# Kernel tuning notes

Measured on AMD Instinct MI355X. Metric: run time of the kernel, lower is better.

Reference implementation:

```python
import jax, jax.numpy as jnp
import numpy as np

N_HEAD = 8
LN_EPS = 1e-6


def setup_inputs() -> dict:
    key = jax.random.key(0)
    ks = jax.random.split(key, 6)
    B, S, D = 4, 2048, 256  # D = hidden_size*2 = input_dim
    sc = 1.0 / np.sqrt(D)
    return {
        "inputs": jax.random.normal(ks[0], (B, S, D), jnp.float32),
        "Wq": jax.random.normal(ks[1], (D, D), jnp.float32) * sc,
        "Wk": jax.random.normal(ks[2], (D, D), jnp.float32) * sc,
        "Wv": jax.random.normal(ks[3], (D, D), jnp.float32) * sc,
        "Wf": jax.random.normal(ks[4], (D, D), jnp.float32) * sc,
        "bf": jnp.zeros((D,), jnp.float32),
        "gamma": jnp.ones((D,), jnp.float32),
        "beta": jnp.zeros((D,), jnp.float32),
    }


def reference(inputs, Wq, Wk, Wv, Wf, bf, gamma, beta):
    B, S, D = inputs.shape
    H = N_HEAD
    dh = D // H
    # Projections (torch Linear: x @ W.T), no bias for Q/K/V
    Q = (inputs @ Wq.T).reshape(B, S, H, dh)
    K = (inputs @ Wk.T).reshape(B, S, H, dh)
    V = (inputs @ Wv.T).reshape(B, S, H, dh)
    # NOTE: original scales by sqrt(K.shape[1]) == sqrt(seq_len), not sqrt(dh)
    scale = 1.0 / jnp.sqrt(jnp.float32(S)).astype(inputs.dtype)
    scores = jnp.einsum("bqhd,bkhd->bhqk", Q, K) * scale  # [B,H,S,S]
    attn = jax.nn.softmax(scores, axis=-1)
    out = jnp.einsum("bhqk,bkhd->bqhd", attn, V).reshape(B, S, D)
    out = out @ Wf.T + bf
    # residual + LayerNorm(eps=1e-6)
    x = inputs + out
    mu = jnp.mean(x, axis=-1, keepdims=True)
    var = jnp.mean(jnp.square(x - mu), axis=-1, keepdims=True)
    return (x - mu) * jax.lax.rsqrt(var + LN_EPS) * gamma + beta
```

## Files before the change

### kernel.cpp

```cpp
#include <hip/hip_runtime.h>
#include <hip/hip_bf16.h>

typedef __attribute__((ext_vector_type(8))) short short8;
typedef __attribute__((ext_vector_type(4))) float f32x4;
typedef __attribute__((ext_vector_type(16))) float f32x16;

#define DEVI __device__ __forceinline__

DEVI unsigned short f2bf(float f) {
  union { float f; unsigned int u; } v; v.f = f;
  unsigned int r = v.u + 0x7fffu + ((v.u >> 16) & 1u);
  return (unsigned short)(r >> 16);
}

#define SB 4
#define SS 2048
#define SD 256
#define SH 8
#define SDH 32
#define SM 8192

#define QSCALE 0.0318793654f

#define XBF_OFF 0
#define W_OFF   (SM * SD)
#define Q_OFF   (W_OFF + 4 * SD * SD)
#define K_OFF   (Q_OFF + SM * SD)
#define VT_OFF  (K_OFF + SM * SD)
#define AO_OFF  (VT_OFF + SM * SD)

__global__ __launch_bounds__(256) void convert_k(
    const float* __restrict__ X, const float* __restrict__ Wq,
    const float* __restrict__ Wk, const float* __restrict__ Wv,
    const float* __restrict__ Wf, unsigned short* __restrict__ ws) {
  const int XN = SM * SD;
  const int WN = SD * SD;
  int i4 = (blockIdx.x * 256 + threadIdx.x) * 4;
  const float* src; unsigned short* dst; int idx;
  if (i4 < XN)             { src = X;  dst = ws + XBF_OFF;      idx = i4; }
  else if (i4 < XN + WN)   { src = Wq; dst = ws + W_OFF;        idx = i4 - XN; }
  else if (i4 < XN + 2*WN) { src = Wk; dst = ws + W_OFF + WN;   idx = i4 - XN - WN; }
  else if (i4 < XN + 3*WN) { src = Wv; dst = ws + W_OFF + 2*WN; idx = i4 - XN - 2*WN; }
  else if (i4 < XN + 4*WN) { src = Wf; dst = ws + W_OFF + 3*WN; idx = i4 - XN - 3*WN; }
  else return;
  float4 v = *reinterpret_cast<const float4*>(src + idx);
  unsigned short o[4] = { f2bf(v.x), f2bf(v.y), f2bf(v.z), f2bf(v.w) };
  *reinterpret_cast<uint2*>(dst + idx) = *reinterpret_cast<const uint2*>(o);
}

__global__ __launch_bounds__(256) void qkv_k(const unsigned short* __restrict__ ws_c,
                                             unsigned short* __restrict__ ws) {
  __shared__ __align__(16) unsigned short Atile[128][72];
  __shared__ __align__(16) unsigned short Btile[128][72];
  const unsigned short* Xb = ws_c + XBF_OFF;
  const unsigned short* Wall = ws_c + W_OFF;
  int tid = threadIdx.x, w = tid >> 6, lane = tid & 63, g = lane >> 4, r = lane & 15;
  int m0 = blockIdx.x * 128, n0 = blockIdx.y * 128;
  int wr = (w >> 1) * 64, wc = (w & 1) * 64;
  f32x4 acc[4][4] = {};
  int srow = tid >> 3, scol = (tid & 7) * 8;
  for (int k0 = 0; k0 < SD; k0 += 64) {
    short8 a[4], b[4];
#pragma unroll
    for (int p = 0; p < 4; ++p) {
      a[p] = *reinterpret_cast<const short8*>(Xb + (m0 + srow + p * 32) * SD + k0 + scol);
      b[p] = *reinterpret_cast<const short8*>(Wall + (n0 + srow + p * 32) * SD + k0 + scol);
    }
    __syncthreads();
#pragma unroll
    for (int p = 0; p < 4; ++p) {
      *reinterpret_cast<short8*>(&Atile[srow + p * 32][scol]) = a[p];
      *reinterpret_cast<short8*>(&Btile[srow + p * 32][scol]) = b[p];
    }
    __syncthreads();
#pragma unroll
    for (int ks = 0; ks < 2; ++ks) {
      short8 af[4], bf[4];
#pragma unroll
      for (int i = 0; i < 4; ++i)
        af[i] = *reinterpret_cast<const short8*>(&Atile[wr + i * 16 + r][ks * 32 + g * 8]);
#pragma unroll
      for (int j = 0; j < 4; ++j)
        bf[j] = *reinterpret_cast<const short8*>(&Btile[wc + j * 16 + r][ks * 32 + g * 8]);
#pragma unroll
      for (int i = 0; i < 4; ++i)
#pragma unroll
        for (int j = 0; j < 4; ++j)
          acc[i][j] = __builtin_amdgcn_mfma_f32_16x16x32_bf16(af[i], bf[j], acc[i][j], 0, 0, 0);
    }
  }
  int z = n0 >> 8;
  int nbase = n0 & 255;
  if (z < 2) {
    unsigned short* out = ws + (z == 0 ? Q_OFF : K_OFF);
    float qs = (z == 0) ? QSCALE : 1.0f;
#pragma unroll
    for (int j = 0; j < 4; ++j) {
      int col = nbase + wc + j * 16 + r;
      int h = col >> 5, d = col & 31;
#pragma unroll
      for (int i = 0; i < 4; ++i) {
#pragma unroll
        for (int jj = 0; jj < 4; ++jj) {
          int m = m0 + wr + i * 16 + g * 4 + jj;
          int b_ = m >> 11, s = m & 2047;
          out[(((b_ << 3) + h) * SS + s) * SDH + d] = f2bf(acc[i][j][jj] * qs);
        }
      }
    }
  } else {
    unsigned short* out = ws + VT_OFF;
#pragma unroll
    for (int j = 0; j < 4; ++j) {
      int col = nbase + wc + j * 16 + r;
      int h = col >> 5, d = col & 31;
#pragma unroll
      for (int i = 0; i < 4; ++i) {
        int m = m0 + wr + i * 16 + g * 4;
        int b_ = m >> 11, s = m & 2047;
        unsigned short o4[4];
#pragma unroll
        for (int jj = 0; jj < 4; ++jj) o4[jj] = f2bf(acc[i][j][jj]);
        *reinterpret_cast<uint2*>(out + ((((b_ << 3) + h) << 5) + d) * SS + s) =
            *reinterpret_cast<const uint2*>(o4);
      }
    }
  }
}

#define TKV 128
__global__ __launch_bounds__(512, 4) void attn_k(const unsigned short* __restrict__ ws_c,
                                                 unsigned short* __restrict__ ws) {
  __shared__ __align__(16) unsigned short Kl[2][TKV][40];
  __shared__ __align__(16) unsigned short Vl[2][32][TKV + 8];
  __shared__ float OC[4][64][16];
  __shared__ float LC[4][64];
  __shared__ float Linv[4][32];
  int tid = threadIdx.x, w = tid >> 6, lane = tid & 63;
  int wg = w >> 2, wl = w & 3, gtid = tid & 255;
  int n32 = lane & 31, hi = lane >> 5;
  int wgid = ((blockIdx.x & 7) << 6) + (blockIdx.x >> 3);
  int bh = wgid >> 4, qb = wgid & 15;
  int q0 = qb * 128 + wl * 32;
  const unsigned short* Qh = ws_c + Q_OFF + bh * (SS * SDH);
  const unsigned short* Kg = ws_c + K_OFF + bh * (SS * SDH) + wg * 1024 * SDH;
  const unsigned short* Vg = ws_c + VT_OFF + bh * (SDH * SS) + wg * 1024;
  short8 qB0 = *reinterpret_cast<const short8*>(Qh + (q0 + n32) * SDH + 8 * hi);
  short8 qB1 = *reinterpret_cast<const short8*>(Qh + (q0 + n32) * SDH + 16 + 8 * hi);
  int krow = gtid >> 2, kcol = (gtid & 3) * 8;
  int vrow = gtid >> 4, vcol = (gtid & 15) * 8;
  f32x16 O = {};
  float Lacc = 0.f;
  short8 ka = *reinterpret_cast<const short8*>(Kg + krow * SDH + kcol);
  short8 kb = *reinterpret_cast<const short8*>(Kg + (64 + krow) * SDH + kcol);
  short8 va = *reinterpret_cast<const short8*>(Vg + vrow * SS + vcol);
  short8 vb = *reinterpret_cast<const short8*>(Vg + (16 + vrow) * SS + vcol);
  for (int t = 0; t < 8; ++t) {
    __syncthreads();
    *reinterpret_cast<short8*>(&Kl[wg][krow][kcol]) = ka;
    *reinterpret_cast<short8*>(&Kl[wg][64 + krow][kcol]) = kb;
    *reinterpret_cast<short8*>(&Vl[wg][vrow][vcol]) = va;
    *reinterpret_cast<short8*>(&Vl[wg][16 + vrow][vcol]) = vb;
    __syncthreads();
    if (t < 7) {
      ka = *reinterpret_cast<const short8*>(Kg + ((t + 1) * TKV + krow) * SDH + kcol);
      kb = *reinterpret_cast<const short8*>(Kg + ((t + 1) * TKV + 64 + krow) * SDH + kcol);
      va = *reinterpret_cast<const short8*>(Vg + vrow * SS + (t + 1) * TKV + vcol);
      vb = *reinterpret_cast<const short8*>(Vg + (16 + vrow) * SS + (t + 1) * TKV + vcol);
    }
#pragma unroll
    for (int s = 0; s < 4; ++s) {
      short8 kA0 = *reinterpret_cast<const short8*>(&Kl[wg][s * 32 + n32][8 * hi]);
      short8 kA1 = *reinterpret_cast<const short8*>(&Kl[wg][s * 32 + n32][16 + 8 * hi]);
      short8 vB0 = *reinterpret_cast<const short8*>(&Vl[wg][n32][s * 32 + 8 * hi]);
      short8 vB1 = *reinterpret_cast<const short8*>(&Vl[wg][n32][s * 32 + 16 + 8 * hi]);
      f32x16 acc = {};
      __builtin_amdgcn_s_setprio(1);
      acc = __builtin_amdgcn_mfma_f32_32x32x16_bf16(kA0, qB0, acc, 0, 0, 0);
      acc = __builtin_amdgcn_mfma_f32_32x32x16_bf16(kA1, qB1, acc, 0, 0, 0);
      __builtin_amdgcn_s_setprio(0);
      float p[16];
#pragma unroll
      for (int i = 0; i < 16; ++i) p[i] = __builtin_amdgcn_exp2f(acc[i]);
      float s0 = 0.f, s1 = 0.f;
#pragma unroll
      for (int i = 0; i < 8; ++i) { s0 += p[2 * i]; s1 += p[2 * i + 1]; }
      Lacc += s0 + s1;
      unsigned int pk[8];
#pragma unroll
      for (int i = 0; i < 8; ++i) {
        unsigned int rr;
        asm("v_cvt_pk_bf16_f32 %0, %1, %2" : "=v"(rr) : "v"(p[2 * i]), "v"(p[2 * i + 1]));
        pk[i] = rr;
      }
      asm("v_permlane32_swap_b32 %0, %1" : "+v"(pk[0]), "+v"(pk[2]));
      asm("v_permlane32_swap_b32 %0, %1" : "+v"(pk[1]), "+v"(pk[3]));
      asm("v_permlane32_swap_b32 %0, %1" : "+v"(pk[4]), "+v"(pk[6]));
      asm("v_permlane32_swap_b32 %0, %1" : "+v"(pk[5]), "+v"(pk[7]));
      union { unsigned int u[4]; short8 sv; } A1, A2;
      A1.u[0] = pk[0]; A1.u[1] = pk[1]; A1.u[2] = pk[2]; A1.u[3] = pk[3];
      A2.u[0] = pk[4]; A2.u[1] = pk[5]; A2.u[2] = pk[6]; A2.u[3] = pk[7];
      __builtin_amdgcn_s_setprio(1);
      O = __builtin_amdgcn_mfma_f32_32x32x16_bf16(A1.sv, vB0, O, 0, 0, 0);
      O = __builtin_amdgcn_mfma_f32_32x32x16_bf16(A2.sv, vB1, O, 0, 0, 0);
      __builtin_amdgcn_s_setprio(0);
    }
  }
  if (wg == 1) {
#pragma unroll
    for (int i = 0; i < 16; ++i) OC[wl][lane][i] = O[i];
    LC[wl][lane] = Lacc;
  }
  __syncthreads();
  if (wg == 0) {
#pragma unroll
    for (int i = 0; i < 16; ++i) O[i] += OC[wl][lane][i];
    Lacc += LC[wl][lane];
    float Lt = Lacc + __shfl_xor(Lacc, 32);
    if (lane < 32) Linv[wl][n32] = 1.0f / Lt;
    int b = bh >> 3, h = bh & 7;
    unsigned short* AO = ws + AO_OFF;
#pragma unroll
    for (int rr = 0; rr < 16; ++rr) {
      int q = (rr & 3) + 8 * (rr >> 2) + 4 * hi;
      AO[(b * SS + q0 + q) * SD + h * SDH + n32] = f2bf(O[rr] * Linv[wl][q]);
    }
  }
}

__global__ __launch_bounds__(256) void final_k(
    const unsigned short* __restrict__ ws_c, const float* __restrict__ X,
    const float* __restrict__ bfv, const float* __restrict__ gamma,
    const float* __restrict__ beta, float* __restrict__ out) {
  __shared__ __align__(16) unsigned short Al[32][72];
  __shared__ __align__(16) unsigned short Bl[256][72];
  __shared__ float Cl[32][257];
  const unsigned short* AO = ws_c + AO_OFF;
  const unsigned short* Wf = ws_c + W_OFF + 3 * (SD * SD);
  int tid = threadIdx.x, w = tid >> 6, lane = tid & 63, g = lane >> 4, r = lane & 15;
  int m0 = blockIdx.x * 32;
  f32x4 acc[2][4] = {};
  int arow = tid >> 3, acol = (tid & 7) * 8;
  for (int k0 = 0; k0 < SD; k0 += 64) {
    short8 av = *reinterpret_cast<const short8*>(AO + (m0 + arow) * SD + k0 + acol);
    short8 bv[8];
#pragma unroll
    for (int i = 0; i < 8; i++)
      bv[i] = *reinterpret_cast<const short8*>(Wf + (i * 32 + arow) * SD + k0 + acol);
    __syncthreads();
    *reinterpret_cast<short8*>(&Al[arow][acol]) = av;
#pragma unroll
    for (int i = 0; i < 8; i++)
      *reinterpret_cast<short8*>(&Bl[i * 32 + arow][acol]) = bv[i];
    __syncthreads();
#pragma unroll
    for (int ks = 0; ks < 2; ks++) {
      short8 af0 = *reinterpret_cast<const short8*>(&Al[r][ks * 32 + g * 8]);
      short8 af1 = *reinterpret_cast<const short8*>(&Al[16 + r][ks * 32 + g * 8]);
#pragma unroll
      for (int nt = 0; nt < 4; nt++) {
        short8 bb = *reinterpret_cast<const short8*>(&Bl[w * 64 + nt * 16 + r][ks * 32 + g * 8]);
        acc[0][nt] = __builtin_amdgcn_mfma_f32_16x16x32_bf16(af0, bb, acc[0][nt], 0, 0, 0);
        acc[1][nt] = __builtin_amdgcn_mfma_f32_16x16x32_bf16(af1, bb, acc[1][nt], 0, 0, 0);
      }
    }
  }
#pragma unroll
  for (int rt = 0; rt < 2; rt++)
#pragma unroll
    for (int nt = 0; nt < 4; nt++)
#pragma unroll
      for (int j = 0; j < 4; j++)
        Cl[rt * 16 + g * 4 + j][w * 64 + nt * 16 + r] = acc[rt][nt][j];
  __syncthreads();
  int row = tid >> 3, sub = tid & 7;
  int m = m0 + row;
  float x[32];
  float sum = 0.f, sumsq = 0.f;
#pragma unroll
  for (int i = 0; i < 8; i++) {
    int col = sub * 32 + i * 4;
    float4 xv = *reinterpret_cast<const float4*>(X + m * SD + col);
    float4 bb = *reinterpret_cast<const float4*>(bfv + col);
    x[i * 4 + 0] = Cl[row][col + 0] + xv.x + bb.x;
    x[i * 4 + 1] = Cl[row][col + 1] + xv.y + bb.y;
    x[i * 4 + 2] = Cl[row][col + 2] + xv.z + bb.z;
    x[i * 4 + 3] = Cl[row][col + 3] + xv.w + bb.w;
  }
#pragma unroll
  for (int c = 0; c < 32; c++) { sum += x[c]; sumsq += x[c] * x[c]; }
  sum += __shfl_xor(sum, 1);  sumsq += __shfl_xor(sumsq, 1);
  sum += __shfl_xor(sum, 2);  sumsq += __shfl_xor(sumsq, 2);
  sum += __shfl_xor(sum, 4);  sumsq += __shfl_xor(sumsq, 4);
  float mean = sum * (1.0f / 256.0f);
  float var = sumsq * (1.0f / 256.0f) - mean * mean;
  float rstd = rsqrtf(var + 1e-6f);
#pragma unroll
  for (int i = 0; i < 8; i++) {
    int col = sub * 32 + i * 4;
    float4 gv = *reinterpret_cast<const float4*>(gamma + col);
    float4 bv2 = *reinterpret_cast<const float4*>(beta + col);
    float4 ov;
    ov.x = (x[i * 4 + 0] - mean) * rstd * gv.x + bv2.x;
    ov.y = (x[i * 4 + 1] - mean) * rstd * gv.y + bv2.y;
    ov.z = (x[i * 4 + 2] - mean) * rstd * gv.z + bv2.z;
    ov.w = (x[i * 4 + 3] - mean) * rstd * gv.w + bv2.w;
    *reinterpret_cast<float4*>(out + m * SD + col) = ov;
  }
}

extern "C" void kernel_launch(void* const* d_in, const int* in_sizes, int n_in,
                              void* d_out, int out_size, void* d_ws, size_t ws_size,
                              hipStream_t stream) {
  const float* X  = (const float*)d_in[0];
  const float* Wq = (const float*)d_in[1];
  const float* Wk = (const float*)d_in[2];
  const float* Wv = (const float*)d_in[3];
  const float* Wf = (const float*)d_in[4];
  const float* bf = (const float*)d_in[5];
  const float* gm = (const float*)d_in[6];
  const float* bt = (const float*)d_in[7];
  float* out = (float*)d_out;
  unsigned short* ws = (unsigned short*)d_ws;

  convert_k<<<2304, 256, 0, stream>>>(X, Wq, Wk, Wv, Wf, ws);
  qkv_k<<<dim3(64, 6), 256, 0, stream>>>(ws, ws);
  attn_k<<<dim3(512), 512, 0, stream>>>(ws, ws);
  final_k<<<256, 256, 0, stream>>>(ws, X, bf, gm, bt, out);
}
```

Before: 60.23 us.

## Stream K/V tiles directly to LDS with async loads and XOR swizzle

Attention now uses global_load_lds to copy K and V tiles straight into double-buffered, XOR-swizzled shared memory, in 64-key tiles with waitcnt/barrier pipelining instead of register staging. The goal is to cut VGPR pressure, avoid the register-to-LDS store and bank conflicts, and overlap the next tile's load with compute. The reduction scratch reuses the K/V buffers to shrink LDS per block. The QKV GEMM also gets a register prefetch of the next k-slice. The risks are more barriers per tile and a correctness dependence on the swizzle and lane-to-LDS mapping of global_load_lds.

```diff
diff --git a/kernel.cpp b/kernel.cpp
--- a/kernel.cpp
+++ b/kernel.cpp
@@ -12,6 +12,11 @@
   unsigned int r = v.u + 0x7fffu + ((v.u >> 16) & 1u);
   return (unsigned short)(r >> 16);
 }
+
+#define GLDS16(gp, lp)                                                         \
+  __builtin_amdgcn_global_load_lds(                                            \
+      (const __attribute__((address_space(1))) unsigned int*)(uintptr_t)(gp),  \
+      (__attribute__((address_space(3))) unsigned int*)(uintptr_t)(lp), 16, 0, 0)
 
 #define SB 4
 #define SS 2048
@@ -59,13 +64,13 @@
   int wr = (w >> 1) * 64, wc = (w & 1) * 64;
   f32x4 acc[4][4] = {};
   int srow = tid >> 3, scol = (tid & 7) * 8;
+  short8 a[4], b[4];
+#pragma unroll
+  for (int p = 0; p < 4; ++p) {
+    a[p] = *reinterpret_cast<const short8*>(Xb + (m0 + srow + p * 32) * SD + scol);
+    b[p] = *reinterpret_cast<const short8*>(Wall + (n0 + srow + p * 32) * SD + scol);
+  }
   for (int k0 = 0; k0 < SD; k0 += 64) {
-    short8 a[4], b[4];
-#pragma unroll
-    for (int p = 0; p < 4; ++p) {
-      a[p] = *reinterpret_cast<const short8*>(Xb + (m0 + srow + p * 32) * SD + k0 + scol);
-      b[p] = *reinterpret_cast<const short8*>(Wall + (n0 + srow + p * 32) * SD + k0 + scol);
-    }
     __syncthreads();
 #pragma unroll
     for (int p = 0; p < 4; ++p) {
@@ -73,6 +78,13 @@
       *reinterpret_cast<short8*>(&Btile[srow + p * 32][scol]) = b[p];
     }
     __syncthreads();
+    if (k0 + 64 < SD) {
+#pragma unroll
+      for (int p = 0; p < 4; ++p) {
+        a[p] = *reinterpret_cast<const short8*>(Xb + (m0 + srow + p * 32) * SD + k0 + 64 + scol);
+        b[p] = *reinterpret_cast<const short8*>(Wall + (n0 + srow + p * 32) * SD + k0 + 64 + scol);
+      }
+    }
 #pragma unroll
     for (int ks = 0; ks < 2; ++ks) {
       short8 af[4], bf[4];
@@ -128,14 +140,10 @@
   }
 }
 
-#define TKV 128
 __global__ __launch_bounds__(512, 4) void attn_k(const unsigned short* __restrict__ ws_c,
                                                  unsigned short* __restrict__ ws) {
-  __shared__ __align__(16) unsigned short Kl[2][TKV][40];
-  __shared__ __align__(16) unsigned short Vl[2][32][TKV + 8];
-  __shared__ float OC[4][64][16];
-  __shared__ float LC[4][64];
-  __shared__ float Linv[4][32];
+  __shared__ __align__(16) unsigned short Kb[2][2][64 * 32];
+  __shared__ __align__(16) unsigned short Vb[2][2][32 * 64];
   int tid = threadIdx.x, w = tid >> 6, lane = tid & 63;
   int wg = w >> 2, wl = w & 3, gtid = tid & 255;
   int n32 = lane & 31, hi = lane >> 5;
@@ -143,54 +151,55 @@
   int bh = wgid >> 4, qb = wgid & 15;
   int q0 = qb * 128 + wl * 32;
   const unsigned short* Qh = ws_c + Q_OFF + bh * (SS * SDH);
-  const unsigned short* Kg = ws_c + K_OFF + bh * (SS * SDH) + wg * 1024 * SDH;
+  const unsigned short* Kg = ws_c + K_OFF + (bh * SS + wg * 1024) * SDH;
   const unsigned short* Vg = ws_c + VT_OFF + bh * (SDH * SS) + wg * 1024;
   short8 qB0 = *reinterpret_cast<const short8*>(Qh + (q0 + n32) * SDH + 8 * hi);
   short8 qB1 = *reinterpret_cast<const short8*>(Qh + (q0 + n32) * SDH + 16 + 8 * hi);
-  int krow = gtid >> 2, kcol = (gtid & 3) * 8;
-  int vrow = gtid >> 4, vcol = (gtid & 15) * 8;
+  int krow = gtid >> 2, kch = (gtid & 3) ^ (krow & 3);
+  const unsigned short* gK = Kg + krow * SDH + kch * 8;
+  int vrow = gtid >> 3, vch = (gtid & 7) ^ (vrow & 7);
+  const unsigned short* gV = Vg + vrow * SS + vch * 8;
+  int wv = gtid >> 6;
+  unsigned short* lK[2] = { &Kb[wg][0][wv * 512], &Kb[wg][1][wv * 512] };
+  unsigned short* lV[2] = { &Vb[wg][0][wv * 512], &Vb[wg][1][wv * 512] };
+  GLDS16(gK, lK[0]);
+  GLDS16(gV, lV[0]);
   f32x16 O = {};
   float Lacc = 0.f;
-  short8 ka = *reinterpret_cast<const short8*>(Kg + krow * SDH + kcol);
-  short8 kb = *reinterpret_cast<const short8*>(Kg + (64 + krow) * SDH + kcol);
-  short8 va = *reinterpret_cast<const short8*>(Vg + vrow * SS + vcol);
-  short8 vb = *reinterpret_cast<const short8*>(Vg + (16 + vrow) * SS + vcol);
-  for (int t = 0; t < 8; ++t) {
-    __syncthreads();
-    *reinterpret_cast<short8*>(&Kl[wg][krow][kcol]) = ka;
-    *reinterpret_cast<short8*>(&Kl[wg][64 + krow][kcol]) = kb;
-    *reinterpret_cast<short8*>(&Vl[wg][vrow][vcol]) = va;
-    *reinterpret_cast<short8*>(&Vl[wg][16 + vrow][vcol]) = vb;
-    __syncthreads();
-    if (t < 7) {
-      ka = *reinterpret_cast<const short8*>(Kg + ((t + 1) * TKV + krow) * SDH + kcol);
-      kb = *reinterpret_cast<const short8*>(Kg + ((t + 1) * TKV + 64 + krow) * SDH + kcol);
-      va = *reinterpret_cast<const short8*>(Vg + vrow * SS + (t + 1) * TKV + vcol);
-      vb = *reinterpret_cast<const short8*>(Vg + (16 + vrow) * SS + (t + 1) * TKV + vcol);
-    }
-#pragma unroll
-    for (int s = 0; s < 4; ++s) {
-      short8 kA0 = *reinterpret_cast<const short8*>(&Kl[wg][s * 32 + n32][8 * hi]);
-      short8 kA1 = *reinterpret_cast<const short8*>(&Kl[wg][s * 32 + n32][16 + 8 * hi]);
-      short8 vB0 = *reinterpret_cast<const short8*>(&Vl[wg][n32][s * 32 + 8 * hi]);
-      short8 vB1 = *reinterpret_cast<const short8*>(&Vl[wg][n32][s * 32 + 16 + 8 * hi]);
+  for (int t = 0; t < 16; ++t) {
+    const unsigned short* Kbase = &Kb[wg][t & 1][0];
+    const unsigned short* Vbase = &Vb[wg][t & 1][0];
+    if (t < 15) {
+      GLDS16(gK + (t + 1) * 64 * SDH, lK[(t + 1) & 1]);
+      GLDS16(gV + (t + 1) * 64, lV[(t + 1) & 1]);
+      asm volatile("s_waitcnt vmcnt(2)" ::: "memory");
+    } else {
+      asm volatile("s_waitcnt vmcnt(0)" ::: "memory");
+    }
+    __builtin_amdgcn_s_barrier();
+#pragma unroll
+    for (int s = 0; s < 2; ++s) {
+      int R0 = s * 32 + n32;
+      short8 kA0 = *reinterpret_cast<const short8*>(Kbase + R0 * 32 + ((hi ^ (n32 & 3)) * 8));
+      short8 kA1 = *reinterpret_cast<const short8*>(Kbase + R0 * 32 + (((2 + hi) ^ (n32 & 3)) * 8));
+      short8 vB0 = *reinterpret_cast<const short8*>(Vbase + n32 * 64 + (((s * 4 + hi) ^ (n32 & 7)) * 8));
+      short8 vB1 = *reinterpret_cast<const short8*>(Vbase + n32 * 64 + (((s * 4 + 2 + hi) ^ (n32 & 7)) * 8));
       f32x16 acc = {};
       __builtin_amdgcn_s_setprio(1);
       acc = __builtin_amdgcn_mfma_f32_32x32x16_bf16(kA0, qB0, acc, 0, 0, 0);
       acc = __builtin_amdgcn_mfma_f32_32x32x16_bf16(kA1, qB1, acc, 0, 0, 0);
       __builtin_amdgcn_s_setprio(0);
-      float p[16];
-#pragma unroll
-      for (int i = 0; i < 16; ++i) p[i] = __builtin_amdgcn_exp2f(acc[i]);
+#pragma unroll
+      for (int i = 0; i < 16; ++i) acc[i] = __builtin_amdgcn_exp2f(acc[i]);
       float s0 = 0.f, s1 = 0.f;
 #pragma unroll
-      for (int i = 0; i < 8; ++i) { s0 += p[2 * i]; s1 += p[2 * i + 1]; }
+      for (int i = 0; i < 8; ++i) { s0 += acc[2 * i]; s1 += acc[2 * i + 1]; }
       Lacc += s0 + s1;
       unsigned int pk[8];
 #pragma unroll
       for (int i = 0; i < 8; ++i) {
         unsigned int rr;
-        asm("v_cvt_pk_bf16_f32 %0, %1, %2" : "=v"(rr) : "v"(p[2 * i]), "v"(p[2 * i + 1]));
+        asm("v_cvt_pk_bf16_f32 %0, %1, %2" : "=v"(rr) : "v"(acc[2 * i]), "v"(acc[2 * i + 1]));
         pk[i] = rr;
       }
       asm("v_permlane32_swap_b32 %0, %1" : "+v"(pk[0]), "+v"(pk[2]));
@@ -205,25 +214,30 @@
       O = __builtin_amdgcn_mfma_f32_32x32x16_bf16(A2.sv, vB1, O, 0, 0, 0);
       __builtin_amdgcn_s_setprio(0);
     }
-  }
+    __builtin_amdgcn_s_barrier();
+  }
+  __syncthreads();
+  float* OCp = reinterpret_cast<float*>(&Kb[0][0][0]);
+  float* LCp = reinterpret_cast<float*>(&Vb[0][0][0]);
   if (wg == 1) {
 #pragma unroll
-    for (int i = 0; i < 16; ++i) OC[wl][lane][i] = O[i];
-    LC[wl][lane] = Lacc;
+    for (int i = 0; i < 16; ++i) OCp[(wl * 64 + lane) * 16 + i] = O[i];
+    LCp[wl * 64 + lane] = Lacc;
   }
   __syncthreads();
   if (wg == 0) {
 #pragma unroll
-    for (int i = 0; i < 16; ++i) O[i] += OC[wl][lane][i];
-    Lacc += LC[wl][lane];
+    for (int i = 0; i < 16; ++i) O[i] += OCp[(wl * 64 + lane) * 16 + i];
+    Lacc += LCp[wl * 64 + lane];
     float Lt = Lacc + __shfl_xor(Lacc, 32);
-    if (lane < 32) Linv[wl][n32] = 1.0f / Lt;
+    float* Linv = LCp + 256 + wl * 32;
+    if (lane < 32) Linv[n32] = 1.0f / Lt;
     int b = bh >> 3, h = bh & 7;
     unsigned short* AO = ws + AO_OFF;
 #pragma unroll
     for (int rr = 0; rr < 16; ++rr) {
       int q = (rr & 3) + 8 * (rr >> 2) + 4 * hi;
-      AO[(b * SS + q0 + q) * SD + h * SDH + n32] = f2bf(O[rr] * Linv[wl][q]);
+      AO[(b * SS + q0 + q) * SD + h * SDH + n32] = f2bf(O[rr] * Linv[q]);
     }
   }
 }
```

Measured after the change: 59.43 us. Within noise of the previous version (-1.3%).
